# Optimization experiments

Hardware: AMD Instinct MI355X
Metric: run time of the kernel (lower is better)

Reference implementation:

```python
import jax, jax.numpy as jnp
import numpy as np

N_NODES = 4000
N_EDGES = 4000
D_IN = 20      # data_length
HID = 768      # hidden_dim
OUT = 2        # output_dim


def _lin(k, i, o):
    s = 1.0 / np.sqrt(i)
    return jax.random.uniform(k, (i, o), jnp.float32, -s, s)


def setup_inputs() -> dict:
    key = jax.random.key(0)
    ks = jax.random.split(key, 16)
    T = N_NODES + N_EDGES
    data = jax.random.normal(ks[0], (N_NODES, D_IN), jnp.float32)
    data_mask = jnp.ones((N_NODES,), jnp.float32)  # unused by forward, kept for signature fidelity
    e_adj_matrix = jax.random.uniform(ks[1], (T, T), jnp.float32) * (2.0 / T)
    transition = jax.random.randint(ks[2], (2, N_EDGES), 0, N_NODES)
    # exactly N_EDGES ones interleaved among N_NODES zeros
    inx = jnp.concatenate([jnp.ones((N_EDGES,), jnp.int32), jnp.zeros((N_NODES,), jnp.int32)])
    label_inx_positive = jax.random.permutation(ks[3], inx)
    label_inx = jax.random.randint(ks[4], (T,), 0, OUT)
    mask = jax.random.randint(ks[5], (T,), 0, 2).astype(jnp.float32)
    return {
        'data': data, 'data_mask': data_mask, 'e_adj_matrix': e_adj_matrix,
        'transition': transition, 'label_inx_positive': label_inx_positive,
        'label_inx': label_inx, 'mask': mask,
        'mlp_w1': _lin(ks[6], 6 * D_IN, HID), 'mlp_b1': jnp.zeros((HID,), jnp.float32),
        'mlp_w2': _lin(ks[7], HID, HID), 'mlp_b2': jnp.zeros((HID,), jnp.float32),
        'mlp2_w1': _lin(ks[8], D_IN, HID), 'mlp2_b1': jnp.zeros((HID,), jnp.float32),
        'mlp2_w2': _lin(ks[9], HID, HID), 'mlp2_b2': jnp.zeros((HID,), jnp.float32),
        'gcn_w1': _lin(ks[10], HID, HID), 'gcn_b1': jnp.zeros((HID,), jnp.float32),
        'gcn_w2': _lin(ks[11], HID, OUT), 'gcn_b2': jnp.zeros((OUT,), jnp.float32),
    }


def gen_edge2(x, trans):
    # Vectorized Gen_edge2: e1 = [x[t1], x[t0]]; e2 = [x[t0], x[t1]] iff reverse edge exists; e3 = e1 + e2.
    t0, t1 = trans[0], trans[1]
    n = x.shape[0]
    keys = t0 * n + t1
    rkeys = t1 * n + t0
    sk = jnp.sort(keys)
    pos = jnp.clip(jnp.searchsorted(sk, rkeys), 0, sk.shape[0] - 1)
    has_rev = sk[pos] == rkeys  # [E]
    e1 = jnp.concatenate([x[t1], x[t0]], axis=1)  # [E, 2d]
    e2 = jnp.where(has_rev[:, None], jnp.concatenate([x[t0], x[t1]], axis=1), 0.0)
    return jnp.concatenate([e1, e2, e1 + e2], axis=1)  # [E, 6d]


def dataset_cgraph(n_feat, e_feat, e_inx):
    # Vectorized interleave: pull next edge row where e_inx==1, else next node row.
    m = e_inx == 1
    idx_e = jnp.clip(jnp.cumsum(m.astype(jnp.int32)) - 1, 0, e_feat.shape[0] - 1)
    idx_n = jnp.clip(jnp.cumsum((~m).astype(jnp.int32)) - 1, 0, n_feat.shape[0] - 1)
    return jnp.where(m[:, None], e_feat[idx_e], n_feat[idx_n])  # [N+E, H]


def reference(data, data_mask, e_adj_matrix, transition, label_inx_positive,
              label_inx, mask, mlp_w1, mlp_b1, mlp_w2, mlp_b2,
              mlp2_w1, mlp2_b1, mlp2_w2, mlp2_b2,
              gcn_w1, gcn_b1, gcn_w2, gcn_b2):
    e_feat = gen_edge2(data, transition)                              # [E, 120]
    e_feat = jax.nn.relu(e_feat @ mlp_w1 + mlp_b1) @ mlp_w2 + mlp_b2  # [E, H]
    n_feat = jax.nn.relu(data @ mlp2_w1 + mlp2_b1) @ mlp2_w2 + mlp2_b2  # [N, H]
    x = dataset_cgraph(n_feat, e_feat, label_inx_positive)            # [N+E, H]
    # 2-layer GCN (GcnModel assumed standard: relu(A X W1), then A H W2)
    h1 = jax.nn.relu(e_adj_matrix @ (x @ gcn_w1) + gcn_b1)            # [N+E, H]
    logits = e_adj_matrix @ (h1 @ gcn_w2) + gcn_b2                    # [N+E, OUT]
    logp = jax.nn.log_softmax(logits, axis=-1)
    ce = -jnp.take_along_axis(logp, label_inx[:, None], axis=1)[:, 0]
    loss = jnp.sum(ce * mask) / jnp.maximum(jnp.sum(mask), 1.0)
    return logits, loss, h1
```

## Files before the change

### kernel.cpp

```cpp
#include <hip/hip_runtime.h>
#include <hip/hip_bf16.h>

#define N_NODES 4000
#define N_EDGES 4000
#define T_ALL   8000
#define HID     768

typedef __attribute__((ext_vector_type(8))) short bf16x8;
typedef __attribute__((ext_vector_type(4))) short s16x4;
typedef __attribute__((ext_vector_type(4))) float f32x4;

__device__ __forceinline__ short f2bf(float f) {
    union { float f; unsigned u; } a; a.f = f;
    unsigned u = a.u;
    unsigned r = (u + 0x7fffu + ((u >> 16) & 1u)) >> 16;
    return (short)(r & 0xffffu);
}
__device__ __forceinline__ float bf2f(short s) {
    union { unsigned u; float f; } a;
    a.u = ((unsigned)(unsigned short)s) << 16;
    return a.f;
}
__device__ __forceinline__ void gload_lds16(const void* g, void* l) {
    __builtin_amdgcn_global_load_lds(
        (const __attribute__((address_space(1))) void*)g,
        (__attribute__((address_space(3))) void*)l, 16, 0, 0);
}

__global__ __launch_bounds__(512, 2) void gemm_ring(
    const short* __restrict__ A, const short* __restrict__ BT,
    short* __restrict__ parts, int M, int K, int lda, int ldbt)
{
    __shared__ __align__(16) short As[4][256 * 32];
    __shared__ __align__(16) short Bs[4][256 * 32];
    const int t    = threadIdx.x;
    const int lane = t & 63;
    const int wv   = t >> 6;
    const int wm   = wv >> 2;
    const int wn   = wv & 3;
    const int lrow = lane & 15;
    const int kgrp = lane >> 4;

    const int nwg  = gridDim.x * gridDim.y * gridDim.z;
    int flat = blockIdx.x + gridDim.x * (blockIdx.y + gridDim.y * blockIdx.z);
    int w    = (flat & 7) * (nwg >> 3) + (flat >> 3);
    const int bx = w % 3;
    int rest = w / 3;
    const int by = rest & 31;
    const int bz = rest >> 5;
    const int bm0 = by << 8;
    const int bn0 = bx << 8;

    const int TC = K >> 5;
    const int Z  = gridDim.z;
    const int q  = TC / Z, r = TC % Z;
    const int nt   = q + (bz < r ? 1 : 0);
    const int kbeg = ((bz < r) ? bz * (q + 1) : r * (q + 1) + (bz - r) * q) << 5;

    auto stageA = [&](int tt) {
        const int k0 = kbeg + (tt << 5);
        short* dst = &As[tt & 3][0];
#pragma unroll
        for (int i = 0; i < 2; ++i) {
            int f = t + (i << 9);
            int row = f >> 2, sl = f & 3;
            int ga = bm0 + row; ga = ga < M ? ga : M - 1;
            gload_lds16(A + (size_t)ga * lda + k0 + ((sl ^ ((row >> 1) & 3)) << 3),
                        dst + f * 8);
        }
    };
    auto stageB = [&](int tt) {
        const int k0 = kbeg + (tt << 5);
        short* dst = &Bs[tt & 3][0];
#pragma unroll
        for (int i = 0; i < 2; ++i) {
            int f = t + (i << 9);
            int row = f >> 2, sl = f & 3;
            gload_lds16(BT + (size_t)(bn0 + row) * ldbt + k0 + ((sl ^ ((row >> 1) & 3)) << 3),
                        dst + f * 8);
        }
    };

    f32x4 acc[8][4];
#pragma unroll
    for (int m = 0; m < 8; ++m)
#pragma unroll
        for (int n = 0; n < 4; ++n) acc[m][n] = (f32x4)(0.0f);

    stageA(0); stageB(0);
    stageA(1); stageB(1);
    stageA(2); stageB(2);
    asm volatile("s_waitcnt vmcnt(8)" ::: "memory");
    __builtin_amdgcn_s_barrier();

    for (int tt = 0; tt < nt; ++tt) {
        const short* Ac = &As[tt & 3][0];
        const short* Bc = &Bs[tt & 3][0];
        bf16x8 af0[4], af1[4], bfv[4];
#pragma unroll
        for (int m = 0; m < 4; ++m) {
            int rr = (wm << 7) + (m << 4) + lrow;
            af0[m] = *reinterpret_cast<const bf16x8*>(
                &Ac[(rr << 5) + ((kgrp ^ ((rr >> 1) & 3)) << 3)]);
        }
#pragma unroll
        for (int n = 0; n < 4; ++n) {
            int rr = (wn << 6) + (n << 4) + lrow;
            bfv[n] = *reinterpret_cast<const bf16x8*>(
                &Bc[(rr << 5) + ((kgrp ^ ((rr >> 1) & 3)) << 3)]);
        }
        if (tt + 3 < nt) stageA(tt + 3);
        __builtin_amdgcn_s_barrier();
        __builtin_amdgcn_s_setprio(1);
#pragma unroll
        for (int m = 0; m < 4; ++m)
#pragma unroll
            for (int n = 0; n < 4; ++n)
                acc[m][n] = __builtin_amdgcn_mfma_f32_16x16x32_bf16(
                    af0[m], bfv[n], acc[m][n], 0, 0, 0);
        __builtin_amdgcn_s_setprio(0);
        __builtin_amdgcn_s_barrier();
#pragma unroll
        for (int m = 0; m < 4; ++m) {
            int rr = (wm << 7) + 64 + (m << 4) + lrow;
            af1[m] = *reinterpret_cast<const bf16x8*>(
                &Ac[(rr << 5) + ((kgrp ^ ((rr >> 1) & 3)) << 3)]);
        }
        if (tt + 3 < nt) stageB(tt + 3);
        __builtin_amdgcn_s_barrier();
        __builtin_amdgcn_s_setprio(1);
#pragma unroll
        for (int m = 0; m < 4; ++m)
#pragma unroll
            for (int n = 0; n < 4; ++n)
                acc[4 + m][n] = __builtin_amdgcn_mfma_f32_16x16x32_bf16(
                    af1[m], bfv[n], acc[4 + m][n], 0, 0, 0);
        __builtin_amdgcn_s_setprio(0);
        int rem = nt - tt;
        if (rem > 3)       asm volatile("s_waitcnt vmcnt(8)" ::: "memory");
        else if (rem == 3) asm volatile("s_waitcnt vmcnt(4)" ::: "memory");
        else if (rem == 2) asm volatile("s_waitcnt vmcnt(0)" ::: "memory");
        __builtin_amdgcn_s_barrier();
    }

    short* Cp = parts + (size_t)bz * 6144000;
#pragma unroll
    for (int m = 0; m < 8; ++m) {
        int r0 = bm0 + (wm << 7) + (m << 4) + (kgrp << 2);
#pragma unroll
        for (int n = 0; n < 4; ++n) {
            int col = bn0 + (wn << 6) + (n << 4) + lrow;
#pragma unroll
            for (int j = 0; j < 4; ++j) {
                int rr = r0 + j;
                if (rr < M) Cp[(size_t)rr * 768 + col] = f2bf(acc[m][n][j]);
            }
        }
    }
}

template<int BIAS, int RELU, int OUTBF, int AF32>
__global__ __launch_bounds__(256) void gemm_bf(
    const void* __restrict__ Av, const short* __restrict__ BT,
    const float* __restrict__ bias, void* __restrict__ Cv,
    int M, int N, int K, int lda, int ldbt, int ldc)
{
    __shared__ __align__(16) short As[2][128 * 64];
    __shared__ __align__(16) short Bs[2][128 * 64];
    const int t    = threadIdx.x;
    const int lane = t & 63;
    const int wave = t >> 6;
    const int wr   = (wave >> 1) << 6;
    const int wc   = (wave & 1) << 6;
    const int lrow = lane & 15;
    const int kgrp = lane >> 4;
    const int bm0  = blockIdx.y << 7;
    const int bn0  = blockIdx.x << 7;
    const short* Ab = (const short*)Av;
    const float* Af = (const float*)Av;

    const int nk = K >> 6;

    auto stage = [&](int kt, int buf) {
        const int k0 = kt << 6;
#pragma unroll
        for (int i = 0; i < 4; ++i) {
            int f = t + (i << 8);
            int row = f >> 3, slot = f & 7;
            int gb = bn0 + row; gb = (gb < N) ? gb : (N - 1);
            gload_lds16(BT + (size_t)gb * ldbt + k0 + ((slot ^ (row & 7)) << 3),
                        &Bs[buf][((i << 8) + (wave << 6)) * 8]);
        }
        if constexpr (!AF32) {
#pragma unroll
            for (int i = 0; i < 4; ++i) {
                int f = t + (i << 8);
                int row = f >> 3, slot = f & 7;
                int ga = bm0 + row; ga = (ga < M) ? ga : (M - 1);
                gload_lds16(Ab + (size_t)ga * lda + k0 + ((slot ^ (row & 7)) << 3),
                            &As[buf][((i << 8) + (wave << 6)) * 8]);
            }
        } else {
#pragma unroll
            for (int i = 0; i < 4; ++i) {
                int f = t + (i << 8);
                int row = f >> 3, c8 = f & 7;
                int ga = bm0 + row; ga = (ga < M) ? ga : (M - 1);
                const float* ap = Af + (size_t)ga * lda + k0 + (c8 << 3);
                float4 v0 = *reinterpret_cast<const float4*>(ap);
                float4 v1 = *reinterpret_cast<const float4*>(ap + 4);
                union { bf16x8 v; short s[8]; } u;
                u.s[0] = f2bf(v0.x); u.s[1] = f2bf(v0.y); u.s[2] = f2bf(v0.z); u.s[3] = f2bf(v0.w);
                u.s[4] = f2bf(v1.x); u.s[5] = f2bf(v1.y); u.s[6] = f2bf(v1.z); u.s[7] = f2bf(v1.w);
                *reinterpret_cast<bf16x8*>(&As[buf][row * 64 + ((c8 ^ (row & 7)) << 3)]) = u.v;
            }
        }
    };

    f32x4 acc[4][4];
#pragma unroll
    for (int m = 0; m < 4; ++m)
#pragma unroll
        for (int n = 0; n < 4; ++n) acc[m][n] = (f32x4)(0.0f);

    auto compute = [&](int buf) {
#pragma unroll
        for (int kk = 0; kk < 2; ++kk) {
            bf16x8 af[4], bfv[4];
#pragma unroll
            for (int m = 0; m < 4; ++m) {
                int rr = wr + m * 16 + lrow;
                af[m] = *reinterpret_cast<const bf16x8*>(
                    &As[buf][rr * 64 + (((kk * 4 + kgrp) ^ (rr & 7)) << 3)]);
            }
#pragma unroll
            for (int n = 0; n < 4; ++n) {
                int rr = wc + n * 16 + lrow;
                bfv[n] = *reinterpret_cast<const bf16x8*>(
                    &Bs[buf][rr * 64 + (((kk * 4 + kgrp) ^ (rr & 7)) << 3)]);
            }
#pragma unroll
            for (int m = 0; m < 4; ++m)
#pragma unroll
                for (int n = 0; n < 4; ++n)
                    acc[m][n] = __builtin_amdgcn_mfma_f32_16x16x32_bf16(
                        af[m], bfv[n], acc[m][n], 0, 0, 0);
        }
    };

    if constexpr (!AF32) {
        stage(0, 0);
        if (nk > 1) stage(1, 1);
        for (int kt = 0; kt < nk - 1; ++kt) {
            asm volatile("s_waitcnt vmcnt(8)" ::: "memory");
            __builtin_amdgcn_s_barrier();
            compute(kt & 1);
            __builtin_amdgcn_s_barrier();
            if (kt + 2 < nk) stage(kt + 2, kt & 1);
        }
        asm volatile("s_waitcnt vmcnt(0)" ::: "memory");
        __builtin_amdgcn_s_barrier();
        compute((nk - 1) & 1);
    } else {
        stage(0, 0);
        __syncthreads();
        int cur = 0;
        for (int kt = 0; kt < nk; ++kt) {
            if (kt + 1 < nk) stage(kt + 1, cur ^ 1);
            compute(cur);
            __syncthreads();
            cur ^= 1;
        }
    }

    short* Cb = (short*)Cv;
    float* Cf = (float*)Cv;
#pragma unroll
    for (int m = 0; m < 4; ++m) {
        int rbase = bm0 + wr + m * 16 + kgrp * 4;
#pragma unroll
        for (int n = 0; n < 4; ++n) {
            int col = bn0 + wc + n * 16 + lrow;
            if (col >= N) continue;
            float bv = BIAS ? bias[col] : 0.0f;
#pragma unroll
            for (int j = 0; j < 4; ++j) {
                int rr = rbase + j;
                if (rr < M) {
                    float v = acc[m][n][j] + bv;
                    if (RELU) v = fmaxf(v, 0.0f);
                    if (OUTBF) Cb[(size_t)rr * ldc + col] = f2bf(v);
                    else       Cf[(size_t)rr * ldc + col] = v;
                }
            }
        }
    }
}

template<int RELU>
__global__ __launch_bounds__(256) void gemm_sel(
    const short* __restrict__ A,
    const short* __restrict__ BT1, const short* __restrict__ BT2,
    const float* __restrict__ bias1, const float* __restrict__ bias2,
    short* __restrict__ C, int K)
{
    __shared__ __align__(16) short As[2][128 * 64];
    __shared__ __align__(16) short Bs[2][128 * 64];
    const int t    = threadIdx.x;
    const int lane = t & 63;
    const int wave = t >> 6;
    const int wr   = (wave >> 1) << 6;
    const int wc   = (wave & 1) << 6;
    const int lrow = lane & 15;
    const int kgrp = lane >> 4;
    const int bm0  = blockIdx.y << 7;
    const int bn0  = blockIdx.x << 7;
    const short* BT   = (bm0 < 4096) ? BT1 : BT2;
    const float* bias = (bm0 < 4096) ? bias1 : bias2;
    const int nk = K >> 6;

    auto stage = [&](int kt, int buf) {
        const int k0 = kt << 6;
#pragma unroll
        for (int i = 0; i < 4; ++i) {
            int f = t + (i << 8);
            int row = f >> 3, slot = f & 7;
            gload_lds16(BT + (size_t)(bn0 + row) * K + k0 + ((slot ^ (row & 7)) << 3),
                        &Bs[buf][((i << 8) + (wave << 6)) * 8]);
        }
#pragma unroll
        for (int i = 0; i < 4; ++i) {
            int f = t + (i << 8);
            int row = f >> 3, slot = f & 7;
            gload_lds16(A + (size_t)(bm0 + row) * K + k0 + ((slot ^ (row & 7)) << 3),
                        &As[buf][((i << 8) + (wave << 6)) * 8]);
        }
    };

    f32x4 acc[4][4];
#pragma unroll
    for (int m = 0; m < 4; ++m)
#pragma unroll
        for (int n = 0; n < 4; ++n) acc[m][n] = (f32x4)(0.0f);

    auto compute = [&](int buf) {
#pragma unroll
        for (int kk = 0; kk < 2; ++kk) {
            bf16x8 af[4], bfv[4];
#pragma unroll
            for (int m = 0; m < 4; ++m) {
                int rr = wr + m * 16 + lrow;
                af[m] = *reinterpret_cast<const bf16x8*>(
                    &As[buf][rr * 64 + (((kk * 4 + kgrp) ^ (rr & 7)) << 3)]);
            }
#pragma unroll
            for (int n = 0; n < 4; ++n) {
                int rr = wc + n * 16 + lrow;
                bfv[n] = *reinterpret_cast<const bf16x8*>(
                    &Bs[buf][rr * 64 + (((kk * 4 + kgrp) ^ (rr & 7)) << 3)]);
            }
#pragma unroll
            for (int m = 0; m < 4; ++m)
#pragma unroll
                for (int n = 0; n < 4; ++n)
                    acc[m][n] = __builtin_amdgcn_mfma_f32_16x16x32_bf16(
                        af[m], bfv[n], acc[m][n], 0, 0, 0);
        }
    };

    stage(0, 0);
    if (nk > 1) stage(1, 1);
    for (int kt = 0; kt < nk - 1; ++kt) {
        asm volatile("s_waitcnt vmcnt(8)" ::: "memory");
        __builtin_amdgcn_s_barrier();
        compute(kt & 1);
        __builtin_amdgcn_s_barrier();
        if (kt + 2 < nk) stage(kt + 2, kt & 1);
    }
    asm volatile("s_waitcnt vmcnt(0)" ::: "memory");
    __builtin_amdgcn_s_barrier();
    compute((nk - 1) & 1);

#pragma unroll
    for (int m = 0; m < 4; ++m) {
        int rbase = bm0 + wr + m * 16 + kgrp * 4;
#pragma unroll
        for (int n = 0; n < 4; ++n) {
            int col = bn0 + wc + n * 16 + lrow;
            float bv = bias[col];
#pragma unroll
            for (int j = 0; j < 4; ++j) {
                float v = acc[m][n][j] + bv;
                if (RELU) v = fmaxf(v, 0.0f);
                C[(size_t)(rbase + j) * 768 + col] = f2bf(v);
            }
        }
    }
}

__global__ __launch_bounds__(256) void prep_all(
    const float* __restrict__ data, const int* __restrict__ trans,
    const float* __restrict__ w1, const float* __restrict__ w2,
    const float* __restrict__ w21, const float* __restrict__ w22,
    const float* __restrict__ gw1, const int* __restrict__ einx,
    short* __restrict__ w1T, short* __restrict__ w2T,
    short* __restrict__ w21T, short* __restrict__ w22T,
    short* __restrict__ gw1T, short* __restrict__ estack,
    int* __restrict__ src)
{
    __shared__ float tile[32][33];
    __shared__ int ibuf[512];
    const int blk = blockIdx.x, tid = threadIdx.x;

    if (blk < 2496) {
        if (blk < 384) {
            int i = blk * 256 + tid, n = i >> 7, k = i & 127;
            w1T[i] = (k < 120) ? f2bf(w1[k * 768 + n]) : (short)0;
        } else if (blk < 1344) {
            if (blk < 960) {
                int j = blk - 384, bx = j % 24, by = j / 24;
                int c0 = bx << 5, r0 = by << 5, tx = tid & 31, ty = tid >> 5;
#pragma unroll
                for (int i = ty; i < 32; i += 8)
                    tile[i][tx] = w2[(size_t)(r0 + i) * 768 + c0 + tx];
                __syncthreads();
#pragma unroll
                for (int i = ty; i < 32; i += 8)
                    w2T[(size_t)(c0 + i) * 768 + r0 + tx] = f2bf(tile[tx][i]);
            } else {
                int i = (blk - 960) * 256 + tid, n = i >> 7, k = i & 127;
                w21T[i] = (k < 20) ? f2bf(w21[k * 768 + n]) : (short)0;
            }
        } else if (blk < 1920) {
            int j = blk - 1344, bx = j % 24, by = j / 24;
            int c0 = bx << 5, r0 = by << 5, tx = tid & 31, ty = tid >> 5;
#pragma unroll
            for (int i = ty; i < 32; i += 8)
                tile[i][tx] = w22[(size_t)(r0 + i) * 768 + c0 + tx];
            __syncthreads();
#pragma unroll
            for (int i = ty; i < 32; i += 8)
                w22T[(size_t)(c0 + i) * 768 + r0 + tx] = f2bf(tile[tx][i]);
        } else {
            int j = blk - 1920, bx = j % 24, by = j / 24;
            int c0 = bx << 5, r0 = by << 5, tx = tid & 31, ty = tid >> 5;
#pragma unroll
            for (int i = ty; i < 32; i += 8)
                tile[i][tx] = gw1[(size_t)(r0 + i) * 768 + c0 + tx];
            __syncthreads();
#pragma unroll
            for (int i = ty; i < 32; i += 8)
                gw1T[(size_t)(c0 + i) * 768 + r0 + tx] = f2bf(tile[tx][i]);
        }
    } else if (blk < 6496) {
        int e = blk - 2496;
        int t0 = trans[e], t1 = trans[N_EDGES + e];
        __shared__ int found;
        if (tid == 0) found = 0;
        __syncthreads();
        for (int j = tid; j < N_EDGES; j += 256)
            if (trans[j] == t1 && trans[N_EDGES + j] == t0) found = 1;
        __syncthreads();
        float h = found ? 1.0f : 0.0f;
        short* rp = estack + (size_t)e * 128;
        if (tid < 20) {
            float x0 = data[t0 * 20 + tid];
            float x1 = data[t1 * 20 + tid];
            rp[tid]        = f2bf(x1);
            rp[20 + tid]   = f2bf(x0);
            rp[40 + tid]   = f2bf(h * x0);
            rp[60 + tid]   = f2bf(h * x1);
            rp[80 + tid]   = f2bf(x1 + h * x0);
            rp[100 + tid]  = f2bf(x0 + h * x1);
        } else if (tid < 28) {
            rp[120 + (tid - 20)] = 0;
        }
    } else if (blk < 8496) {
        int i = (blk - 6496) * 256 + tid;
        int r = i >> 7, c = i & 127;
        estack[(size_t)(4096) * 128 + i] = (c < 20) ? f2bf(data[r * 20 + c]) : (short)0;
    } else {
        int* partial = ibuf;
        int* excl    = ibuf + 256;
        int base = tid * 32;
        int cnt = 0;
        for (int i = 0; i < 32; ++i) {
            int idx = base + i;
            if (idx < T_ALL) cnt += (einx[idx] == 1);
        }
        partial[tid] = cnt;
        __syncthreads();
        if (tid == 0) {
            int s = 0;
            for (int i = 0; i < 256; ++i) { excl[i] = s; s += partial[i]; }
        }
        __syncthreads();
        int ce = excl[tid];
        int cn = base - ce;
        for (int i = 0; i < 32; ++i) {
            int idx = base + i;
            if (idx >= T_ALL) break;
            if (einx[idx] == 1) { src[idx] = N_NODES + ce; ce++; }
            else                { src[idx] = cn; cn++; }
        }
    }
}

__global__ __launch_bounds__(192) void reduce_h1_hw(
    const short* __restrict__ p, const float* __restrict__ bias,
    const float* __restrict__ w2, float* __restrict__ h1, float* __restrict__ hw,
    int Z)
{
    int r = blockIdx.x, t = threadIdx.x;
    int c0 = t * 4;
    size_t base = (size_t)r * 768 + c0;
    float a[4];
#pragma unroll
    for (int j = 0; j < 4; ++j) a[j] = bias[c0 + j];
    for (int z = 0; z < Z; ++z) {
        s16x4 v = *reinterpret_cast<const s16x4*>(p + (size_t)z * 6144000 + base);
#pragma unroll
        for (int j = 0; j < 4; ++j) a[j] += bf2f(v[j]);
    }
    float d0 = 0.0f, d1 = 0.0f;
    float4 o;
#pragma unroll
    for (int j = 0; j < 4; ++j) {
        float v = fmaxf(a[j], 0.0f);
        ((float*)&o)[j] = v;
        d0 += v * w2[(c0 + j) * 2];
        d1 += v * w2[(c0 + j) * 2 + 1];
    }
    *reinterpret_cast<float4*>(h1 + base) = o;
#pragma unroll
    for (int off = 32; off > 0; off >>= 1) {
        d0 += __shfl_down(d0, off);
        d1 += __shfl_down(d1, off);
    }
    __shared__ float s0[3], s1[3];
    int wvv = t >> 6, ln = t & 63;
    if (ln == 0) { s0[wvv] = d0; s1[wvv] = d1; }
    __syncthreads();
    if (t == 0) {
        hw[r * 2]     = s0[0] + s0[1] + s0[2];
        hw[r * 2 + 1] = s1[0] + s1[1] + s1[2];
    }
}


__global__ void cvt_bf16(const float* __restrict__ in, short* __restrict__ out, int n8)
{
    int i = blockIdx.x * 256 + threadIdx.x;
    if (i >= n8) return;
    float4 v0 = *reinterpret_cast<const float4*>(in + (size_t)i * 8);
    float4 v1 = *reinterpret_cast<const float4*>(in + (size_t)i * 8 + 4);
    union { bf16x8 v; short s[8]; } u;
    u.s[0] = f2bf(v0.x); u.s[1] = f2bf(v0.y); u.s[2] = f2bf(v0.z); u.s[3] = f2bf(v0.w);
    u.s[4] = f2bf(v1.x); u.s[5] = f2bf(v1.y); u.s[6] = f2bf(v1.z); u.s[7] = f2bf(v1.w);
    *reinterpret_cast<bf16x8*>(out + (size_t)i * 8) = u.v;
}

__global__ void gather_x(const short* __restrict__ nfeat, const short* __restrict__ efeat,
                         const int* __restrict__ src, short* __restrict__ x)
{
    int i = blockIdx.x * 256 + threadIdx.x;
    int r = i / 96, c = i % 96;
    int s = src[r];
    const bf16x8* rowp = (s >= N_NODES)
        ? reinterpret_cast<const bf16x8*>(efeat + (size_t)(s - N_NODES) * HID)
        : reinterpret_cast<const bf16x8*>(nfeat + (size_t)s * HID);
    reinterpret_cast<bf16x8*>(x)[i] = rowp[c];
}

__global__ void h1w2_kernel(const float* __restrict__ h1, const float* __restrict__ w2,
                            float* __restrict__ hw)
{
    int wave = threadIdx.x >> 6, lane = threadIdx.x & 63;
    int row = blockIdx.x * 4 + wave;
    const float* hp = h1 + (size_t)row * HID;
    float a0 = 0.0f, a1 = 0.0f;
    for (int k = lane; k < HID; k += 64) {
        float h = hp[k];
        a0 += h * w2[k * 2];
        a1 += h * w2[k * 2 + 1];
    }
    for (int off = 32; off > 0; off >>= 1) {
        a0 += __shfl_down(a0, off);
        a1 += __shfl_down(a1, off);
    }
    if (lane == 0) { hw[row * 2] = a0; hw[row * 2 + 1] = a1; }
}

__global__ __launch_bounds__(256) void adj_hw_bf(const short* __restrict__ A,
    const float* __restrict__ hw, const float* __restrict__ b2, float* __restrict__ logits)
{
    int row = blockIdx.x;
    const short* ar = A + (size_t)row * T_ALL;
    float a0 = 0.0f, a1 = 0.0f;
    for (int c = threadIdx.x; c < 1000; c += 256) {
        bf16x8 v = *reinterpret_cast<const bf16x8*>(ar + c * 8);
#pragma unroll
        for (int j = 0; j < 8; ++j) {
            float av = bf2f(v[j]);
            int k = c * 8 + j;
            a0 += av * hw[k * 2];
            a1 += av * hw[k * 2 + 1];
        }
    }
    __shared__ float s0[256], s1[256];
    s0[threadIdx.x] = a0; s1[threadIdx.x] = a1;
    __syncthreads();
    for (int o = 128; o > 0; o >>= 1) {
        if (threadIdx.x < o) {
            s0[threadIdx.x] += s0[threadIdx.x + o];
            s1[threadIdx.x] += s1[threadIdx.x + o];
        }
        __syncthreads();
    }
    if (threadIdx.x == 0) {
        logits[row * 2]     = s0[0] + b2[0];
        logits[row * 2 + 1] = s1[0] + b2[1];
    }
}

__global__ __launch_bounds__(256) void adj_hw_f32(const float* __restrict__ A,
    const float* __restrict__ hw, const float* __restrict__ b2, float* __restrict__ logits)
{
    int row = blockIdx.x;
    const float* ar = A + (size_t)row * T_ALL;
    float a0 = 0.0f, a1 = 0.0f;
    for (int k = threadIdx.x; k < T_ALL; k += 256) {
        float v = ar[k];
        a0 += v * hw[k * 2];
        a1 += v * hw[k * 2 + 1];
    }
    __shared__ float s0[256], s1[256];
    s0[threadIdx.x] = a0; s1[threadIdx.x] = a1;
    __syncthreads();
    for (int o = 128; o > 0; o >>= 1) {
        if (threadIdx.x < o) {
            s0[threadIdx.x] += s0[threadIdx.x + o];
            s1[threadIdx.x] += s1[threadIdx.x + o];
        }
        __syncthreads();
    }
    if (threadIdx.x == 0) {
        logits[row * 2]     = s0[0] + b2[0];
        logits[row * 2 + 1] = s1[0] + b2[1];
    }
}

__global__ __launch_bounds__(256) void loss_kernel(const float* __restrict__ logits,
    const int* __restrict__ label, const float* __restrict__ mask, float* __restrict__ outp)
{
    __shared__ float sc[256], sm[256];
    float ac = 0.0f, am = 0.0f;
    for (int i = threadIdx.x; i < T_ALL; i += 256) {
        float l0 = logits[i * 2], l1 = logits[i * 2 + 1];
        float mx = fmaxf(l0, l1);
        float lse = mx + logf(expf(l0 - mx) + expf(l1 - mx));
        float li = label[i] ? l1 : l0;
        ac += (lse - li) * mask[i];
        am += mask[i];
    }
    sc[threadIdx.x] = ac; sm[threadIdx.x] = am;
    __syncthreads();
    for (int o = 128; o > 0; o >>= 1) {
        if (threadIdx.x < o) {
            sc[threadIdx.x] += sc[threadIdx.x + o];
            sm[threadIdx.x] += sm[threadIdx.x + o];
        }
        __syncthreads();
    }
    if (threadIdx.x == 0) *outp = sc[0] / fmaxf(sm[0], 1.0f);
}


extern "C" void kernel_launch(void* const* d_in, const int* in_sizes, int n_in,
                              void* d_out, int out_size, void* d_ws, size_t ws_size,
                              hipStream_t stream)
{
    (void)in_sizes; (void)n_in; (void)out_size;

    const float* data  = (const float*)d_in[0];
    const float* adj   = (const float*)d_in[2];
    const int*   trans = (const int*)d_in[3];
    const int*   einx  = (const int*)d_in[4];
    const int*   label = (const int*)d_in[5];
    const float* mask  = (const float*)d_in[6];
    const float* w1    = (const float*)d_in[7];
    const float* b1    = (const float*)d_in[8];
    const float* w2    = (const float*)d_in[9];
    const float* b2    = (const float*)d_in[10];
    const float* w21   = (const float*)d_in[11];
    const float* b21   = (const float*)d_in[12];
    const float* w22   = (const float*)d_in[13];
    const float* b22   = (const float*)d_in[14];
    const float* gw1   = (const float*)d_in[15];
    const float* gb1   = (const float*)d_in[16];
    const float* gw2   = (const float*)d_in[17];
    const float* gb2   = (const float*)d_in[18];

    char* W = (char*)d_ws;
    short* w1T    = (short*)(W + 0);
    short* w2T    = (short*)(W + 196608);
    short* w21T   = (short*)(W + 1376256);
    short* w22T   = (short*)(W + 1572864);
    short* gw1T   = (short*)(W + 2752512);
    short* estack = (short*)(W + 3932160);
    short* C1s    = (short*)(W + 6029312);
    short* F2s    = (short*)(W + 18612224);
    short* xbuf   = (short*)(W + 31195136);
    int*   hr     = (int*)(W + 43483136);
    int*   src    = (int*)(W + 43499136);
    (void)hr;

    const bool mid  = (ws_size >= (size_t)140352000);
    const bool big2 = (ws_size >= (size_t)189504000);
    const bool big3 = (ws_size >= (size_t)238656000);
    short* adjbf = (short*)W;
    short* xwT;  float* hwbuf;  short* parts = nullptr;
    if (mid) {
        xwT   = (short*)(W + 128000000);
        hwbuf = (float*)(W + 140288000);
        if (big2) parts = (short*)(W + 140352000);
    } else {
        xwT   = (short*)(W + 48425856);
        hwbuf = (float*)(W + 60713856);
    }

    float* out    = (float*)d_out;
    float* logits = out;
    float* lossp  = out + 16000;
    float* h1     = out + 16001;

    prep_all<<<8497, 256, 0, stream>>>(data, trans, w1, w2, w21, w22, gw1, einx,
                                       w1T, w2T, w21T, w22T, gw1T, estack, src);

    gemm_sel<1><<<dim3(6, 64), 256, 0, stream>>>(estack, w1T, w21T, b1, b21, C1s, 128);
    gemm_sel<0><<<dim3(6, 64), 256, 0, stream>>>(C1s, w2T, w22T, b2, b22, F2s, 768);

    gather_x<<<3000, 256, 0, stream>>>(F2s + (size_t)4096 * 768, F2s, src, xbuf);

    gemm_bf<0, 0, 1, 0><<<dim3(63, 6), 256, 0, stream>>>(gw1T, xbuf, nullptr, xwT, 768, 8000, 768, 768, 768, 8000);

    if (mid) {
        cvt_bf16<<<31250, 256, 0, stream>>>(adj, adjbf, 8000000);
        if (big2) {
            const int Z = big3 ? 8 : 4;
            gemm_ring<<<dim3(3, 32, Z), 512, 0, stream>>>(adjbf, xwT, parts, 8000, 8000, 8000, 8000);
            reduce_h1_hw<<<8000, 192, 0, stream>>>(parts, gb1, gw2, h1, hwbuf, Z);
        } else {
            gemm_bf<1, 1, 0, 0><<<dim3(6, 63), 256, 0, stream>>>(adjbf, xwT, gb1, h1, 8000, 768, 8000, 8000, 8000, 768);
            h1w2_kernel<<<2000, 256, 0, stream>>>(h1, gw2, hwbuf);
        }
        adj_hw_bf<<<8000, 256, 0, stream>>>(adjbf, hwbuf, gb2, logits);
    } else {
        gemm_bf<1, 1, 0, 1><<<dim3(6, 63), 256, 0, stream>>>(adj, xwT, gb1, h1, 8000, 768, 8000, 8000, 8000, 768);
        h1w2_kernel<<<2000, 256, 0, stream>>>(h1, gw2, hwbuf);
        adj_hw_f32<<<8000, 256, 0, stream>>>(adj, hwbuf, gb2, logits);
    }
    loss_kernel<<<1, 256, 0, stream>>>(logits, label, mask, lossp);
}
```

Before: 334.3 us.

## Double-buffer LDS fragments in registers and cut barriers in bf16 GEMM loop

```diff
diff --git a/kernel.cpp b/kernel.cpp
--- a/kernel.cpp
+++ b/kernel.cpp
@@ -90,58 +90,88 @@
     stageA(0); stageB(0);
     stageA(1); stageB(1);
     stageA(2); stageB(2);
-    asm volatile("s_waitcnt vmcnt(8)" ::: "memory");
+    asm volatile("s_waitcnt vmcnt(4)" ::: "memory");
     __builtin_amdgcn_s_barrier();
 
-    for (int tt = 0; tt < nt; ++tt) {
-        const short* Ac = &As[tt & 3][0];
-        const short* Bc = &Bs[tt & 3][0];
-        bf16x8 af0[4], af1[4], bfv[4];
+    bf16x8 r0A0[4], r0A1[4], r0B[4];
+    bf16x8 r1A0[4], r1A1[4], r1B[4];
+
+    {
+        const short* Ac = &As[0][0];
+        const short* Bc = &Bs[0][0];
 #pragma unroll
         for (int m = 0; m < 4; ++m) {
             int rr = (wm << 7) + (m << 4) + lrow;
-            af0[m] = *reinterpret_cast<const bf16x8*>(
+            r0A0[m] = *reinterpret_cast<const bf16x8*>(
                 &Ac[(rr << 5) + ((kgrp ^ ((rr >> 1) & 3)) << 3)]);
         }
 #pragma unroll
         for (int n = 0; n < 4; ++n) {
             int rr = (wn << 6) + (n << 4) + lrow;
-            bfv[n] = *reinterpret_cast<const bf16x8*>(
+            r0B[n] = *reinterpret_cast<const bf16x8*>(
                 &Bc[(rr << 5) + ((kgrp ^ ((rr >> 1) & 3)) << 3)]);
         }
-        if (tt + 3 < nt) stageA(tt + 3);
-        __builtin_amdgcn_s_barrier();
-        __builtin_amdgcn_s_setprio(1);
-#pragma unroll
-        for (int m = 0; m < 4; ++m)
-#pragma unroll
-            for (int n = 0; n < 4; ++n)
-                acc[m][n] = __builtin_amdgcn_mfma_f32_16x16x32_bf16(
-                    af0[m], bfv[n], acc[m][n], 0, 0, 0);
-        __builtin_amdgcn_s_setprio(0);
-        __builtin_amdgcn_s_barrier();
 #pragma unroll
         for (int m = 0; m < 4; ++m) {
             int rr = (wm << 7) + 64 + (m << 4) + lrow;
-            af1[m] = *reinterpret_cast<const bf16x8*>(
+            r0A1[m] = *reinterpret_cast<const bf16x8*>(
                 &Ac[(rr << 5) + ((kgrp ^ ((rr >> 1) & 3)) << 3)]);
         }
-        if (tt + 3 < nt) stageB(tt + 3);
-        __builtin_amdgcn_s_barrier();
-        __builtin_amdgcn_s_setprio(1);
-#pragma unroll
-        for (int m = 0; m < 4; ++m)
-#pragma unroll
-            for (int n = 0; n < 4; ++n)
-                acc[4 + m][n] = __builtin_amdgcn_mfma_f32_16x16x32_bf16(
-                    af1[m], bfv[n], acc[4 + m][n], 0, 0, 0);
-        __builtin_amdgcn_s_setprio(0);
-        int rem = nt - tt;
-        if (rem > 3)       asm volatile("s_waitcnt vmcnt(8)" ::: "memory");
-        else if (rem == 3) asm volatile("s_waitcnt vmcnt(4)" ::: "memory");
-        else if (rem == 2) asm volatile("s_waitcnt vmcnt(0)" ::: "memory");
-        __builtin_amdgcn_s_barrier();
-    }
+    }
+
+#define TILE_STEP(TT, cA0, cA1, cB, nA0, nA1, nB)                              \
+    {                                                                          \
+        const int _tt = (TT);                                                  \
+        if (_tt + 1 < nt) {                                                    \
+            const short* An = &As[(_tt + 1) & 3][0];                           \
+            const short* Bn = &Bs[(_tt + 1) & 3][0];                           \
+            _Pragma("unroll")                                                  \
+            for (int m = 0; m < 4; ++m) {                                      \
+                int rr = (wm << 7) + (m << 4) + lrow;                          \
+                nA0[m] = *reinterpret_cast<const bf16x8*>(                     \
+                    &An[(rr << 5) + ((kgrp ^ ((rr >> 1) & 3)) << 3)]);         \
+            }                                                                  \
+            _Pragma("unroll")                                                  \
+            for (int n = 0; n < 4; ++n) {                                      \
+                int rr = (wn << 6) + (n << 4) + lrow;                          \
+                nB[n] = *reinterpret_cast<const bf16x8*>(                      \
+                    &Bn[(rr << 5) + ((kgrp ^ ((rr >> 1) & 3)) << 3)]);         \
+            }                                                                  \
+            _Pragma("unroll")                                                  \
+            for (int m = 0; m < 4; ++m) {                                      \
+                int rr = (wm << 7) + 64 + (m << 4) + lrow;                     \
+                nA1[m] = *reinterpret_cast<const bf16x8*>(                     \
+                    &An[(rr << 5) + ((kgrp ^ ((rr >> 1) & 3)) << 3)]);         \
+            }                                                                  \
+        }                                                                      \
+        if (_tt + 3 < nt) { stageA(_tt + 3); stageB(_tt + 3); }                \
+        __builtin_amdgcn_sched_barrier(0);                                     \
+        __builtin_amdgcn_s_setprio(1);                                         \
+        _Pragma("unroll")                                                      \
+        for (int m = 0; m < 4; ++m)                                            \
+            _Pragma("unroll")                                                  \
+            for (int n = 0; n < 4; ++n)                                        \
+                acc[m][n] = __builtin_amdgcn_mfma_f32_16x16x32_bf16(           \
+                    cA0[m], cB[n], acc[m][n], 0, 0, 0);                        \
+        _Pragma("unroll")                                                      \
+        for (int m = 0; m < 4; ++m)                                            \
+            _Pragma("unroll")                                                  \
+            for (int n = 0; n < 4; ++n)                                        \
+                acc[4 + m][n] = __builtin_amdgcn_mfma_f32_16x16x32_bf16(       \
+                    cA1[m], cB[n], acc[4 + m][n], 0, 0, 0);                    \
+        __builtin_amdgcn_s_setprio(0);                                         \
+        if (_tt <= nt - 4) asm volatile("s_waitcnt vmcnt(4)" ::: "memory");    \
+        else               asm volatile("s_waitcnt vmcnt(0)" ::: "memory");    \
+        __builtin_amdgcn_s_barrier();                                          \
+    }
+
+    int tt = 0;
+    for (; tt + 1 < nt; tt += 2) {
+        TILE_STEP(tt,     r0A0, r0A1, r0B, r1A0, r1A1, r1B);
+        TILE_STEP(tt + 1, r1A0, r1A1, r1B, r0A0, r0A1, r0B);
+    }
+    if (tt < nt) TILE_STEP(tt, r0A0, r0A1, r0B, r1A0, r1A1, r1B);
+#undef TILE_STEP
 
     short* Cp = parts + (size_t)bz * 6144000;
 #pragma unroll
@@ -711,9 +741,7 @@
     short* C1s    = (short*)(W + 6029312);
     short* F2s    = (short*)(W + 18612224);
     short* xbuf   = (short*)(W + 31195136);
-    int*   hr     = (int*)(W + 43483136);
     int*   src    = (int*)(W + 43499136);
-    (void)hr;
 
     const bool mid  = (ws_size >= (size_t)140352000);
     const bool big2 = (ws_size >= (size_t)189504000);
```

After: 325.3 us. -2.7%, faster.

## Replace 4-stage LDS ring with 2-stage double buffer in split-K GEMM

Applied to the files above, without the earlier changes.

```diff
diff --git a/kernel.cpp b/kernel.cpp
--- a/kernel.cpp
+++ b/kernel.cpp
@@ -31,8 +31,8 @@
     const short* __restrict__ A, const short* __restrict__ BT,
     short* __restrict__ parts, int M, int K, int lda, int ldbt)
 {
-    __shared__ __align__(16) short As[4][256 * 32];
-    __shared__ __align__(16) short Bs[4][256 * 32];
+    __shared__ __align__(16) short As[2][256 * 32];
+    __shared__ __align__(16) short Bs[2][256 * 32];
     const int t    = threadIdx.x;
     const int lane = t & 63;
     const int wv   = t >> 6;
@@ -59,7 +59,7 @@
 
     auto stageA = [&](int tt) {
         const int k0 = kbeg + (tt << 5);
-        short* dst = &As[tt & 3][0];
+        short* dst = &As[tt & 1][0];
 #pragma unroll
         for (int i = 0; i < 2; ++i) {
             int f = t + (i << 9);
@@ -71,7 +71,7 @@
     };
     auto stageB = [&](int tt) {
         const int k0 = kbeg + (tt << 5);
-        short* dst = &Bs[tt & 3][0];
+        short* dst = &Bs[tt & 1][0];
 #pragma unroll
         for (int i = 0; i < 2; ++i) {
             int f = t + (i << 9);
@@ -88,19 +88,21 @@
         for (int n = 0; n < 4; ++n) acc[m][n] = (f32x4)(0.0f);
 
     stageA(0); stageB(0);
-    stageA(1); stageB(1);
-    stageA(2); stageB(2);
-    asm volatile("s_waitcnt vmcnt(8)" ::: "memory");
-    __builtin_amdgcn_s_barrier();
+    if (nt > 1) { stageA(1); stageB(1); }
 
     for (int tt = 0; tt < nt; ++tt) {
-        const short* Ac = &As[tt & 3][0];
-        const short* Bc = &Bs[tt & 3][0];
-        bf16x8 af0[4], af1[4], bfv[4];
-#pragma unroll
-        for (int m = 0; m < 4; ++m) {
+        if (tt + 1 < nt) asm volatile("s_waitcnt vmcnt(4)" ::: "memory");
+        else             asm volatile("s_waitcnt vmcnt(0)" ::: "memory");
+        __builtin_amdgcn_sched_barrier(0);
+        __builtin_amdgcn_s_barrier();
+
+        const short* Ac = &As[tt & 1][0];
+        const short* Bc = &Bs[tt & 1][0];
+        bf16x8 af[8], bfv[4];
+#pragma unroll
+        for (int m = 0; m < 8; ++m) {
             int rr = (wm << 7) + (m << 4) + lrow;
-            af0[m] = *reinterpret_cast<const bf16x8*>(
+            af[m] = *reinterpret_cast<const bf16x8*>(
                 &Ac[(rr << 5) + ((kgrp ^ ((rr >> 1) & 3)) << 3)]);
         }
 #pragma unroll
@@ -109,38 +111,17 @@
             bfv[n] = *reinterpret_cast<const bf16x8*>(
                 &Bc[(rr << 5) + ((kgrp ^ ((rr >> 1) & 3)) << 3)]);
         }
-        if (tt + 3 < nt) stageA(tt + 3);
-        __builtin_amdgcn_s_barrier();
         __builtin_amdgcn_s_setprio(1);
 #pragma unroll
-        for (int m = 0; m < 4; ++m)
+        for (int m = 0; m < 8; ++m)
 #pragma unroll
             for (int n = 0; n < 4; ++n)
                 acc[m][n] = __builtin_amdgcn_mfma_f32_16x16x32_bf16(
-                    af0[m], bfv[n], acc[m][n], 0, 0, 0);
+                    af[m], bfv[n], acc[m][n], 0, 0, 0);
         __builtin_amdgcn_s_setprio(0);
         __builtin_amdgcn_s_barrier();
-#pragma unroll
-        for (int m = 0; m < 4; ++m) {
-            int rr = (wm << 7) + 64 + (m << 4) + lrow;
-            af1[m] = *reinterpret_cast<const bf16x8*>(
-                &Ac[(rr << 5) + ((kgrp ^ ((rr >> 1) & 3)) << 3)]);
-        }
-        if (tt + 3 < nt) stageB(tt + 3);
-        __builtin_amdgcn_s_barrier();
-        __builtin_amdgcn_s_setprio(1);
-#pragma unroll
-        for (int m = 0; m < 4; ++m)
-#pragma unroll
-            for (int n = 0; n < 4; ++n)
-                acc[4 + m][n] = __builtin_amdgcn_mfma_f32_16x16x32_bf16(
-                    af1[m], bfv[n], acc[4 + m][n], 0, 0, 0);
-        __builtin_amdgcn_s_setprio(0);
-        int rem = nt - tt;
-        if (rem > 3)       asm volatile("s_waitcnt vmcnt(8)" ::: "memory");
-        else if (rem == 3) asm volatile("s_waitcnt vmcnt(4)" ::: "memory");
-        else if (rem == 2) asm volatile("s_waitcnt vmcnt(0)" ::: "memory");
-        __builtin_amdgcn_s_barrier();
+
+        if (tt + 2 < nt) { stageA(tt + 2); stageB(tt + 2); }
     }
 
     short* Cp = parts + (size_t)bz * 6144000;
@@ -711,9 +692,7 @@
     short* C1s    = (short*)(W + 6029312);
     short* F2s    = (short*)(W + 18612224);
     short* xbuf   = (short*)(W + 31195136);
-    int*   hr     = (int*)(W + 43483136);
     int*   src    = (int*)(W + 43499136);
-    (void)hr;
 
     const bool mid  = (ws_size >= (size_t)140352000);
     const bool big2 = (ws_size >= (size_t)189504000);
```

Result: slower. 348.1 us (+4.1%).
